# Optimization experiments

Hardware: AMD Instinct MI355X
Metric: run time of the kernel (lower is better)

Reference implementation:

```python
import jax, jax.numpy as jnp
import numpy as np

B, S, H, R, K, L = 8, 2048, 512, 7, 10, 4
OFFSETS = np.array([-3, -2, -1, 1, 2, 3], dtype=np.int32)
BN_EPS = 1e-5


def setup_inputs() -> dict:
    key = jax.random.key(0)
    ks = jax.random.split(key, 12)
    u = lambda k, shape, s: jax.random.uniform(k, shape, minval=-s, maxval=s, dtype=jnp.float32)
    s3, sh, shr = 1.0 / np.sqrt(3.0), 1.0 / np.sqrt(H), 1.0 / np.sqrt(R * H)
    return {
        "n_coords": jax.random.normal(ks[0], (B, S, 3), jnp.float32),
        "ca_coords": jax.random.normal(ks[1], (B, S, 3), jnp.float32),
        "c_coords": jax.random.normal(ks[2], (B, S, 3), jnp.float32),
        "Wp": u(ks[3], (H, 3), s3),
        "bp": u(ks[4], (H,), s3),
        "Wlin": u(ks[5], (L, H, R * H), shr),
        "blin": u(ks[6], (L, H), shr),
        "Wself": u(ks[7], (L, H, H), sh),
        "bself": u(ks[8], (L, H), sh),
        "bn_gamma": jnp.ones((L, H), jnp.float32),
        "bn_beta": jnp.zeros((L, H), jnp.float32),
        "bn_mean": jax.random.normal(ks[9], (L, H), jnp.float32) * 0.1,
        "bn_var": jax.random.uniform(ks[10], (L, H), minval=0.5, maxval=1.5, dtype=jnp.float32),
    }


def _edges(pos):
    """Edge list per graph: sequential offsets -3..3 -> relations 0..5, KNN(k=10) -> relation 6."""
    i = jnp.arange(S)
    off = jnp.asarray(OFFSETS)
    dst_seq = i[:, None] + off[None, :]                            # [S,6]
    valid = (dst_seq >= 0) & (dst_seq < S)
    src_seq = jnp.broadcast_to(i[:, None], (S, 6))
    rel_seq = jnp.broadcast_to(jnp.arange(6, dtype=jnp.int32)[None, :], (S, 6))
    dst_seq = jnp.clip(dst_seq, 0, S - 1)
    # squared distances give the same topk-smallest ordering as torch.norm
    d2 = jnp.sum((pos[:, None, :] - pos[None, :, :]) ** 2, axis=-1)  # [S,S]
    _, knn = jax.lax.top_k(-d2, K + 1)                             # k+1 smallest, self first
    dst_knn = knn[:, 1:]                                           # drop self
    src_knn = jnp.broadcast_to(i[:, None], (S, K))
    rel_knn = jnp.full((S, K), 6, dtype=jnp.int32)
    src = jnp.concatenate([src_seq.reshape(-1), src_knn.reshape(-1)])
    dst = jnp.concatenate([dst_seq.reshape(-1), dst_knn.reshape(-1)])
    rel = jnp.concatenate([rel_seq.reshape(-1), rel_knn.reshape(-1)])
    w = jnp.concatenate([valid.reshape(-1).astype(pos.dtype),
                         jnp.ones((S * K,), pos.dtype)])
    return src, dst, rel, w


def _gearnet(ca_coords, Wp, bp, Wlin, blin, Wself, bself, bn_gamma, bn_beta, bn_mean, bn_var):
    def per_graph(pos):
        src, dst, rel, w = _edges(pos)
        seg = dst * R + rel                                        # node_out*num_relation + relation
        h = pos @ Wp.T + bp                                        # coord_projection: Linear(3, H)
        for l in range(L):
            msg = h[src] * w[:, None]                              # [E,H] gather + edge weight
            upd = jax.ops.segment_sum(msg, seg, num_segments=S * R)  # scatter-add per (node, relation)
            upd = upd.reshape(S, R * H)
            out = upd @ Wlin[l].T + blin[l] + h @ Wself[l].T + bself[l]
            out = (out - bn_mean[l]) * jax.lax.rsqrt(bn_var[l] + BN_EPS) * bn_gamma[l] + bn_beta[l]
            h = jax.nn.relu(out) + h                               # relu then short_cut residual
        return h
    return jax.vmap(per_graph)(ca_coords)                          # [B,S,H]


def reference(n_coords, ca_coords, c_coords, Wp, bp, Wlin, blin, Wself, bself,
              bn_gamma, bn_beta, bn_mean, bn_var):
    # n_coords / c_coords are accepted but unused, exactly as in the original forward.
    return _gearnet(ca_coords, Wp, bp, Wlin, blin, Wself, bself,
                    bn_gamma, bn_beta, bn_mean, bn_var)
```

## Files before the change

### kernel.cpp

```cpp
#include <hip/hip_runtime.h>
#include <stdint.h>

#define B_ 8
#define S_ 2048
#define H_ 512
#define R_ 7
#define K_ 10
#define L_ 4
#define KT_ 4096
#define RH_ 3584

typedef __attribute__((ext_vector_type(8))) short bf16x8;
typedef __attribute__((ext_vector_type(4))) float f32x4;
typedef __attribute__((ext_vector_type(4))) unsigned short u16x4;
typedef unsigned long long u64;

__device__ __forceinline__ unsigned short f2bf(float f){
  unsigned int u = __float_as_uint(f);
  u = (u + 0x7fffu + ((u >> 16) & 1u)) >> 16;
  return (unsigned short)u;
}

__device__ __forceinline__ float bf2f(unsigned short s){
  return __uint_as_float(((unsigned int)s) << 16);
}

__device__ __forceinline__ f32x4 bf4load(const unsigned short* p){
  u16x4 v = *(const u16x4*)p;
  f32x4 o;
#pragma unroll
  for (int e = 0; e < 4; e++) o[e] = bf2f(v[e]);
  return o;
}

__device__ __forceinline__ void gload16(const void* g, void* lds){
  __builtin_amdgcn_global_load_lds(
      (const __attribute__((address_space(1))) unsigned int*)g,
      (__attribute__((address_space(3))) unsigned int*)lds, 16, 0, 0);
}

__global__ __launch_bounds__(256) void knn_kernel(const float* __restrict__ pos,
                                                  int* __restrict__ knn){
  __shared__ float4 p4[S_];
  int b = blockIdx.y;
  const float* p = pos + (size_t)b * S_ * 3;
  for (int idx = threadIdx.x; idx < S_; idx += 256){
    float4 v; v.x = p[idx*3+0]; v.y = p[idx*3+1]; v.z = p[idx*3+2]; v.w = 0.f;
    p4[idx] = v;
  }
  __syncthreads();
  int w = threadIdx.x >> 6, l = threadIdx.x & 63;
  int i = blockIdx.x * 4 + w;
  float4 pi = p4[i];
  float xi = pi.x, yi = pi.y, zi = pi.z;
  u64 best[6];
#pragma unroll
  for (int q = 0; q < 6; q++) best[q] = ~0ull;
#pragma unroll 1
  for (int j = l; j < S_; j += 64){
    if (j == i) continue;
    float4 pj = p4[j];
    float dx = __fsub_rn(xi, pj.x);
    float dy = __fsub_rn(yi, pj.y);
    float dz = __fsub_rn(zi, pj.z);
    float d2 = __fadd_rn(__fadd_rn(__fmul_rn(dx,dx), __fmul_rn(dy,dy)), __fmul_rn(dz,dz));
    u64 key = ((u64)__float_as_uint(d2) << 32) | (unsigned)j;
    if (key < best[5]){
      best[5] = key;
#pragma unroll
      for (int q = 5; q > 0; --q){
        u64 a = best[q-1], c = best[q];
        u64 lo = a < c ? a : c, hi = a < c ? c : a;
        best[q-1] = lo; best[q] = hi;
      }
    }
  }
  int* out = knn + ((size_t)b * S_ + i) * K_;
#pragma unroll
  for (int t = 0; t < 10; t++){
    u64 cand = best[0];
    u64 m = cand;
#pragma unroll
    for (int o = 32; o; o >>= 1){
      u64 other = __shfl_xor(m, o);
      if (other < m) m = other;
    }
    if (cand == m){
#pragma unroll
      for (int q = 0; q < 5; q++) best[q] = best[q+1];
      best[5] = ~0ull;
    }
    if (l == 0) out[t] = (int)(unsigned)(m & 0xffffffffu);
  }
}

__global__ void count_kernel(const int* __restrict__ knn, int* __restrict__ counts){
  int idx = blockIdx.x * 256 + threadIdx.x;
  int b = idx / (S_ * K_);
  int d = knn[idx];
  atomicAdd(&counts[b * S_ + d], 1);
}

__global__ __launch_bounds__(256) void scan_kernel(const int* __restrict__ counts,
                                                   int* __restrict__ row_start,
                                                   int* __restrict__ cursor){
  __shared__ int lds[256];
  int b = blockIdx.x, t = threadIdx.x;
  int base = b * S_;
  int v[8]; int s = 0;
#pragma unroll
  for (int e = 0; e < 8; e++){ v[e] = s; s += counts[base + t*8 + e]; }
  lds[t] = s;
  __syncthreads();
  int total = s;
  for (int o = 1; o < 256; o <<= 1){
    int add = 0;
    if (t >= o) add = lds[t - o];
    __syncthreads();
    lds[t] += add;
    __syncthreads();
  }
  int ex = lds[t] - total;
  int rb = b * (S_ + 1);
#pragma unroll
  for (int e = 0; e < 8; e++){
    int val = ex + v[e];
    row_start[rb + t*8 + e] = val;
    cursor[base + t*8 + e] = val;
  }
  if (t == 255) row_start[rb + S_] = lds[255];
}

__global__ void fill_kernel(const int* __restrict__ knn, int* __restrict__ cursor,
                            int* __restrict__ col){
  int idx = blockIdx.x * 256 + threadIdx.x;
  int b = idx / (S_ * K_);
  int i = (idx / K_) % S_;
  int d = knn[idx];
  int p = atomicAdd(&cursor[b * S_ + d], 1);
  col[(size_t)b * S_ * K_ + p] = i;
}

__global__ void sort_kernel(const int* __restrict__ row_start, int* __restrict__ col){
  int idx = blockIdx.x * 256 + threadIdx.x;
  int b = idx / S_, d = idx % S_;
  int rs = row_start[b*(S_+1)+d], re = row_start[b*(S_+1)+d+1];
  int* c = col + (size_t)b * S_ * K_;
  for (int a = rs + 1; a < re; ++a){
    int vv = c[a]; int q = a - 1;
    while (q >= rs && c[q] > vv){ c[q+1] = c[q]; --q; }
    c[q+1] = vv;
  }
}

__global__ void prepw_kernel(const float* __restrict__ Wlin, const float* __restrict__ Wself,
                             unsigned short* __restrict__ Wt){
  size_t e = ((size_t)blockIdx.x * 256 + threadIdx.x) * 8;
  int k = (int)(e & 4095);
  int j = (int)((e >> 12) & 511);
  int l = (int)(e >> 21);
  const float* src = (k < RH_) ? Wlin + ((size_t)l * H_ + j) * RH_ + k
                               : Wself + ((size_t)l * H_ + j) * H_ + (k - RH_);
  union { unsigned short s[8]; uint4 u; } pk;
#pragma unroll
  for (int t = 0; t < 8; t++) pk.s[t] = f2bf(src[t]);
  *(uint4*)&Wt[e] = pk.u;
}

__global__ void prepa_kernel(const float* __restrict__ gam, const float* __restrict__ bet,
                             const float* __restrict__ mean, const float* __restrict__ var,
                             const float* __restrict__ blin, const float* __restrict__ bself,
                             float* __restrict__ scale, float* __restrict__ shift){
  int idx = blockIdx.x * 256 + threadIdx.x;
  float sc = gam[idx] * rsqrtf(var[idx] + 1e-5f);
  scale[idx] = sc;
  shift[idx] = bet[idx] + (blin[idx] + bself[idx] - mean[idx]) * sc;
}

__global__ void inith_kernel(const float* __restrict__ pos, const float* __restrict__ Wp,
                             const float* __restrict__ bp, float* __restrict__ h,
                             unsigned short* __restrict__ hb){
  int idx = blockIdx.x * 256 + threadIdx.x;
  int j = (idx & 127) * 4;
  int bs = idx >> 7;
  const float* p = pos + (size_t)bs * 3;
  float x = p[0], y = p[1], z = p[2];
  f32x4 o;
#pragma unroll
  for (int e = 0; e < 4; e++){
    const float* wr = Wp + (j + e) * 3;
    o[e] = x * wr[0] + y * wr[1] + z * wr[2] + bp[j + e];
  }
  *(f32x4*)&h[(size_t)bs * H_ + j] = o;
  unsigned int w0 = f2bf(o[0]) | ((unsigned)f2bf(o[1]) << 16);
  unsigned int w1 = f2bf(o[2]) | ((unsigned)f2bf(o[3]) << 16);
  uint2 u; u.x = w0; u.y = w1;
  *(uint2*)&hb[(size_t)bs * H_ + j] = u;
}

__global__ __launch_bounds__(256) void hknn_kernel(const unsigned short* __restrict__ hb,
                                                   const int* __restrict__ row_start,
                                                   const int* __restrict__ col,
                                                   unsigned short* __restrict__ hk){
  int w = threadIdx.x >> 6, l = threadIdx.x & 63;
  int d = blockIdx.x * 4 + w;
  int b = blockIdx.y;
  int rs = row_start[b * (S_ + 1) + d];
  int re = row_start[b * (S_ + 1) + d + 1];
  const int* cl = col + (size_t)b * S_ * K_;
  const unsigned short* base = hb + (size_t)b * S_ * H_ + l * 8;
  f32x4 aLo = {0,0,0,0}, aHi = {0,0,0,0}, bLo = {0,0,0,0}, bHi = {0,0,0,0};
  int e = rs;
  for (; e + 1 < re; e += 2){
    uint4 v0 = *(const uint4*)(base + (size_t)cl[e]     * H_);
    uint4 v1 = *(const uint4*)(base + (size_t)cl[e + 1] * H_);
    aLo[0] += __uint_as_float(v0.x << 16); aLo[1] += __uint_as_float(v0.x & 0xffff0000u);
    aLo[2] += __uint_as_float(v0.y << 16); aLo[3] += __uint_as_float(v0.y & 0xffff0000u);
    aHi[0] += __uint_as_float(v0.z << 16); aHi[1] += __uint_as_float(v0.z & 0xffff0000u);
    aHi[2] += __uint_as_float(v0.w << 16); aHi[3] += __uint_as_float(v0.w & 0xffff0000u);
    bLo[0] += __uint_as_float(v1.x << 16); bLo[1] += __uint_as_float(v1.x & 0xffff0000u);
    bLo[2] += __uint_as_float(v1.y << 16); bLo[3] += __uint_as_float(v1.y & 0xffff0000u);
    bHi[0] += __uint_as_float(v1.z << 16); bHi[1] += __uint_as_float(v1.z & 0xffff0000u);
    bHi[2] += __uint_as_float(v1.w << 16); bHi[3] += __uint_as_float(v1.w & 0xffff0000u);
  }
  if (e < re){
    uint4 v0 = *(const uint4*)(base + (size_t)cl[e] * H_);
    aLo[0] += __uint_as_float(v0.x << 16); aLo[1] += __uint_as_float(v0.x & 0xffff0000u);
    aLo[2] += __uint_as_float(v0.y << 16); aLo[3] += __uint_as_float(v0.y & 0xffff0000u);
    aHi[0] += __uint_as_float(v0.z << 16); aHi[1] += __uint_as_float(v0.z & 0xffff0000u);
    aHi[2] += __uint_as_float(v0.w << 16); aHi[3] += __uint_as_float(v0.w & 0xffff0000u);
  }
  aLo += bLo; aHi += bHi;
  uint4 o;
  o.x = f2bf(aLo[0]) | ((unsigned)f2bf(aLo[1]) << 16);
  o.y = f2bf(aLo[2]) | ((unsigned)f2bf(aLo[3]) << 16);
  o.z = f2bf(aHi[0]) | ((unsigned)f2bf(aHi[1]) << 16);
  o.w = f2bf(aHi[2]) | ((unsigned)f2bf(aHi[3]) << 16);
  *(uint4*)(hk + ((size_t)b * S_ + d) * H_ + l * 8) = o;
}

__global__ __launch_bounds__(512) void gemmf_kernel(
    const unsigned short* __restrict__ hbin,
    const unsigned short* __restrict__ hkn,
    const unsigned short* __restrict__ Wt,
    float* __restrict__ h,
    unsigned short* __restrict__ hbout,
    const float* __restrict__ scale,
    const float* __restrict__ shift,
    const unsigned short* __restrict__ zbuf){
  __shared__ unsigned short As[3][128 * 64];
  __shared__ unsigned short Bs[3][256 * 64];
  int tid = threadIdx.x;
  int wg = blockIdx.x;
  int swz = (wg & 7) * 32 + (wg >> 3);
  int my = swz >> 1;
  int nx = swz & 1;
  int l = tid & 63, wid = tid >> 6;
  int wm = wid >> 2, wn = wid & 3;
  f32x4 acc[4][4] = {};

  int arow = tid >> 3;
  int lA8 = ((tid & 7) ^ (arow & 7)) << 3;
  int gr0 = my * 128 + arow, gr1 = gr0 + 64;
  const unsigned short* Bp0 = Wt + (size_t)(nx * 256 +   0 + arow) * KT_ + lA8;
  const unsigned short* Bp1 = Wt + (size_t)(nx * 256 +  64 + arow) * KT_ + lA8;
  const unsigned short* Bp2 = Wt + (size_t)(nx * 256 + 128 + arow) * KT_ + lA8;
  const unsigned short* Bp3 = Wt + (size_t)(nx * 256 + 192 + arow) * KT_ + lA8;
  const unsigned short *sa0, *sa1;

#define SETSLC(rr) do {                                                       \
    int _r = (rr);                                                            \
    const unsigned short *_b0, *_b1;                                          \
    if (_r < 6){                                                              \
      int _sh = (_r < 3) ? (3 - _r) : (2 - _r);          \
      int _s0 = gr0 + _sh, _s1 = gr1 + _sh;                                   \
      _b0 = (((unsigned)_s0 >> 11) == ((unsigned)gr0 >> 11)) ? hbin + (size_t)_s0 * H_ : zbuf; \
      _b1 = (((unsigned)_s1 >> 11) == ((unsigned)gr1 >> 11)) ? hbin + (size_t)_s1 * H_ : zbuf; \
    } else {                                                                  \
      const unsigned short* _bb = (_r == 6) ? hkn : hbin;                     \
      _b0 = _bb + (size_t)gr0 * H_; _b1 = _bb + (size_t)gr1 * H_;             \
    }                                                                         \
    sa0 = _b0 + lA8; sa1 = _b1 + lA8;                                         \
  } while (0)

  int dA0 = tid * 8, dA1 = (512 + tid) * 8;
  int dB0 = tid * 8, dB1 = (512 + tid) * 8, dB2 = (1024 + tid) * 8, dB3 = (1536 + tid) * 8;

#define STAGE(sl, ko, kb) do {                             \
    gload16(sa0 + (ko), &As[sl][dA0]);                     \
    gload16(sa1 + (ko), &As[sl][dA1]);                     \
    gload16(Bp0 + (kb), &Bs[sl][dB0]);                     \
    gload16(Bp1 + (kb), &Bs[sl][dB1]);                     \
    gload16(Bp2 + (kb), &Bs[sl][dB2]);                     \
    gload16(Bp3 + (kb), &Bs[sl][dB3]);                     \
  } while (0)

  SETSLC(0);
  STAGE(0, 0, 0);
  STAGE(1, 64, 64);
  asm volatile("s_waitcnt vmcnt(6)" ::: "memory");
  __builtin_amdgcn_s_barrier();
  asm volatile("" ::: "memory");

  int kcr = l >> 4, lr = l & 15, lr7 = l & 7;
  int rA0 = wm * 64 + lr, rB0 = wn * 64 + lr;
  int pc0 = (kcr ^ lr7) * 8;
  int pc1 = ((4 + kcr) ^ lr7) * 8;
  int s = 0;
#pragma unroll 1
  for (int t = 0; t < 64; ++t){
    int s2 = s + 2; if (s2 >= 3) s2 -= 3;
    int tt = t + 2;
    bool st = (t < 62);
    if (st) SETSLC(tt >> 3);

    bf16x8 af0[4], af1[4], bf0[4], bf1[4];
#pragma unroll
    for (int mi = 0; mi < 4; mi++)
      af0[mi] = *(const bf16x8*)&As[s][(rA0 + mi * 16) * 64 + pc0];
#pragma unroll
    for (int ni = 0; ni < 4; ni++)
      bf0[ni] = *(const bf16x8*)&Bs[s][(rB0 + ni * 16) * 64 + pc0];
    __builtin_amdgcn_sched_barrier(0);
#pragma unroll
    for (int mi = 0; mi < 4; mi++)
      af1[mi] = *(const bf16x8*)&As[s][(rA0 + mi * 16) * 64 + pc1];
#pragma unroll
    for (int ni = 0; ni < 4; ni++)
      bf1[ni] = *(const bf16x8*)&Bs[s][(rB0 + ni * 16) * 64 + pc1];
    __builtin_amdgcn_sched_barrier(0);

    asm volatile("s_waitcnt lgkmcnt(8)" ::: "memory");
    __builtin_amdgcn_sched_barrier(0);
    __builtin_amdgcn_s_setprio(1);
#pragma unroll
    for (int mi = 0; mi < 4; mi++)
#pragma unroll
      for (int ni = 0; ni < 4; ni++)
        acc[mi][ni] = __builtin_amdgcn_mfma_f32_16x16x32_bf16(af0[mi], bf0[ni], acc[mi][ni], 0, 0, 0);
    __builtin_amdgcn_s_setprio(0);
    __builtin_amdgcn_sched_barrier(0);

    if (st) STAGE(s2, (tt & 7) * 64, tt * 64);

    asm volatile("s_waitcnt lgkmcnt(0)" ::: "memory");
    __builtin_amdgcn_sched_barrier(0);
    __builtin_amdgcn_s_setprio(1);
#pragma unroll
    for (int mi = 0; mi < 4; mi++)
#pragma unroll
      for (int ni = 0; ni < 4; ni++)
        acc[mi][ni] = __builtin_amdgcn_mfma_f32_16x16x32_bf16(af1[mi], bf1[ni], acc[mi][ni], 0, 0, 0);
    __builtin_amdgcn_s_setprio(0);
    asm volatile("" ::: "memory");

    if (t < 62)       asm volatile("s_waitcnt vmcnt(6)" ::: "memory");
    else if (t == 62) asm volatile("s_waitcnt vmcnt(0)" ::: "memory");
    if (t < 63){
      __builtin_amdgcn_s_barrier();
      asm volatile("" ::: "memory");
    }
    ++s; if (s == 3) s = 0;
  }
#undef STAGE
#undef SETSLC

  int r0 = (l >> 4) * 4, c0 = l & 15;
#pragma unroll
  for (int ni = 0; ni < 4; ni++){
    int gcol = nx * 256 + wn * 64 + ni * 16 + c0;
    float sc = scale[gcol], sf = shift[gcol];
#pragma unroll
    for (int mi = 0; mi < 4; mi++){
#pragma unroll
      for (int reg = 0; reg < 4; reg++){
        int grow = my * 128 + wm * 64 + mi * 16 + r0 + reg;
        size_t o = (size_t)grow * H_ + gcol;
        float val = fmaxf(acc[mi][ni][reg] * sc + sf, 0.f);
        float hv = h[o] + val;
        h[o] = hv;
        hbout[o] = f2bf(hv);
      }
    }
  }
}

extern "C" void kernel_launch(void* const* d_in, const int* in_sizes, int n_in,
                              void* d_out, int out_size, void* d_ws, size_t ws_size,
                              hipStream_t stream){
  const float* ca    = (const float*)d_in[1];
  const float* Wp    = (const float*)d_in[3];
  const float* bp    = (const float*)d_in[4];
  const float* Wlin  = (const float*)d_in[5];
  const float* blin  = (const float*)d_in[6];
  const float* Wself = (const float*)d_in[7];
  const float* bself = (const float*)d_in[8];
  const float* gam   = (const float*)d_in[9];
  const float* bet   = (const float*)d_in[10];
  const float* mean  = (const float*)d_in[11];
  const float* var   = (const float*)d_in[12];
  float* h = (float*)d_out;

  char* ws = (char*)d_ws;
  size_t off = 0;
  auto alloc = [&](size_t bytes) -> char* {
    char* p = ws + off;
    off = (off + bytes + 255) & ~(size_t)255;
    return p;
  };
  int* knn       = (int*)alloc((size_t)B_ * S_ * K_ * 4);
  int* counts    = (int*)alloc((size_t)B_ * S_ * 4);
  int* row_start = (int*)alloc((size_t)B_ * (S_ + 1) * 4);
  int* cursor    = (int*)alloc((size_t)B_ * S_ * 4);
  int* col       = (int*)alloc((size_t)B_ * S_ * K_ * 4);
  unsigned short* Wt  = (unsigned short*)alloc((size_t)L_ * H_ * KT_ * 2);
  float* scale   = (float*)alloc((size_t)L_ * H_ * 4);
  float* shift   = (float*)alloc((size_t)L_ * H_ * 4);
  unsigned short* hbA = (unsigned short*)alloc((size_t)B_ * S_ * H_ * 2);
  unsigned short* hbB = (unsigned short*)alloc((size_t)B_ * S_ * H_ * 2);
  unsigned short* hkn = (unsigned short*)alloc((size_t)B_ * S_ * H_ * 2);
  unsigned short* zbuf = (unsigned short*)alloc(4096 * 2);

  hipMemsetAsync(counts, 0, (size_t)B_ * S_ * 4, stream);
  hipMemsetAsync(zbuf, 0, 4096 * 2, stream);
  knn_kernel<<<dim3(S_ / 4, B_), 256, 0, stream>>>(ca, knn);
  count_kernel<<<dim3(B_ * S_ * K_ / 256), 256, 0, stream>>>(knn, counts);
  scan_kernel<<<dim3(B_), 256, 0, stream>>>(counts, row_start, cursor);
  fill_kernel<<<dim3(B_ * S_ * K_ / 256), 256, 0, stream>>>(knn, cursor, col);
  sort_kernel<<<dim3(B_ * S_ / 256), 256, 0, stream>>>(row_start, col);
  prepw_kernel<<<dim3((int)((size_t)L_ * H_ * KT_ / 8 / 256)), 256, 0, stream>>>(Wlin, Wself, Wt);
  prepa_kernel<<<dim3(L_ * H_ / 256), 256, 0, stream>>>(gam, bet, mean, var, blin, bself, scale, shift);
  inith_kernel<<<dim3(B_ * S_ * (H_ / 4) / 256), 256, 0, stream>>>(ca, Wp, bp, h, hbA);

  for (int l = 0; l < L_; l++){
    unsigned short* in  = (l & 1) ? hbB : hbA;
    unsigned short* out = (l & 1) ? hbA : hbB;
    hknn_kernel<<<dim3(S_ / 4, B_), 256, 0, stream>>>(in, row_start, col, hkn);
    gemmf_kernel<<<dim3(256), 512, 0, stream>>>(
        in, hkn, Wt + (size_t)l * H_ * KT_, h, out,
        scale + l * H_, shift + l * H_, zbuf);
  }
}
```

Baseline: 527.3 us.

## Load A operand directly from global into registers, bypassing LDS

The fused GEMM now fetches the A (activation) tile straight from global memory into MFMA fragment registers with inline global_load_dwordx4, double-buffered across tiles, and keeps only the weight tile in shared memory. This drops A writes to and reads from LDS and frees LDS capacity. In exchange, A rows are read redundantly by the four wn waves through cache, register pressure rises, and the load pattern is less coalesced. The zero buffer is enlarged to cover the wider per-lane offsets.

Result: slower. 789.7 us (+49.8%).

```diff
diff --git a/kernel.cpp b/kernel.cpp
--- a/kernel.cpp
+++ b/kernel.cpp
@@ -248,7 +248,6 @@
     const float* __restrict__ scale,
     const float* __restrict__ shift,
     const unsigned short* __restrict__ zbuf){
-  __shared__ unsigned short As[3][128 * 64];
   __shared__ unsigned short Bs[3][256 * 64];
   int tid = threadIdx.x;
   int wg = blockIdx.x;
@@ -261,109 +260,120 @@
 
   int arow = tid >> 3;
   int lA8 = ((tid & 7) ^ (arow & 7)) << 3;
-  int gr0 = my * 128 + arow, gr1 = gr0 + 64;
   const unsigned short* Bp0 = Wt + (size_t)(nx * 256 +   0 + arow) * KT_ + lA8;
   const unsigned short* Bp1 = Wt + (size_t)(nx * 256 +  64 + arow) * KT_ + lA8;
   const unsigned short* Bp2 = Wt + (size_t)(nx * 256 + 128 + arow) * KT_ + lA8;
   const unsigned short* Bp3 = Wt + (size_t)(nx * 256 + 192 + arow) * KT_ + lA8;
-  const unsigned short *sa0, *sa1;
-
-#define SETSLC(rr) do {                                                       \
-    int _r = (rr);                                                            \
-    const unsigned short *_b0, *_b1;                                          \
-    if (_r < 6){                                                              \
-      int _sh = (_r < 3) ? (3 - _r) : (2 - _r);          \
-      int _s0 = gr0 + _sh, _s1 = gr1 + _sh;                                   \
-      _b0 = (((unsigned)_s0 >> 11) == ((unsigned)gr0 >> 11)) ? hbin + (size_t)_s0 * H_ : zbuf; \
-      _b1 = (((unsigned)_s1 >> 11) == ((unsigned)gr1 >> 11)) ? hbin + (size_t)_s1 * H_ : zbuf; \
-    } else {                                                                  \
-      const unsigned short* _bb = (_r == 6) ? hkn : hbin;                     \
-      _b0 = _bb + (size_t)gr0 * H_; _b1 = _bb + (size_t)gr1 * H_;             \
-    }                                                                         \
-    sa0 = _b0 + lA8; sa1 = _b1 + lA8;                                         \
-  } while (0)
-
-  int dA0 = tid * 8, dA1 = (512 + tid) * 8;
   int dB0 = tid * 8, dB1 = (512 + tid) * 8, dB2 = (1024 + tid) * 8, dB3 = (1536 + tid) * 8;
 
-#define STAGE(sl, ko, kb) do {                             \
-    gload16(sa0 + (ko), &As[sl][dA0]);                     \
-    gload16(sa1 + (ko), &As[sl][dA1]);                     \
+#define STAGEB(sl, kb) do {                                \
     gload16(Bp0 + (kb), &Bs[sl][dB0]);                     \
     gload16(Bp1 + (kb), &Bs[sl][dB1]);                     \
     gload16(Bp2 + (kb), &Bs[sl][dB2]);                     \
     gload16(Bp3 + (kb), &Bs[sl][dB3]);                     \
   } while (0)
 
+  int lr = l & 15, kcr = l >> 4, lr7 = l & 7;
+  int graphid = (my * 128) >> 11;
+  const unsigned short* pA[4];
+
+#define SETSLC(rr) do {                                                       \
+    int _r = (rr);                                                            \
+    int _sh = (_r < 6) ? ((_r < 3) ? (3 - _r) : (2 - _r)) : 0;                \
+    const unsigned short* _bb = (_r == 6) ? hkn : hbin;                       \
+    _Pragma("unroll")                                                         \
+    for (int _mi = 0; _mi < 4; _mi++){                                        \
+      int _src = my * 128 + wm * 64 + _mi * 16 + lr + _sh;                    \
+      bool _ok = (_r >= 6) || ((_src >> 11) == graphid);                      \
+      pA[_mi] = (_ok ? _bb + (size_t)_src * H_ : zbuf) + kcr * 8;             \
+    }                                                                         \
+  } while (0)
+
+#define LOADA(A, T) do {                                                      \
+    int _ko = ((T) & 7) * 64;                                                 \
+    _Pragma("unroll")                                                         \
+    for (int _mi = 0; _mi < 4; _mi++){                                        \
+      asm volatile("global_load_dwordx4 %0, %1, off"                          \
+        : "=v"(A[_mi][0]) : "v"(pA[_mi] + _ko) : "memory");                   \
+      asm volatile("global_load_dwordx4 %0, %1, off"                          \
+        : "=v"(A[_mi][1]) : "v"(pA[_mi] + _ko + 32) : "memory");              \
+    }                                                                         \
+  } while (0)
+
+  bf16x8 Ae[4][2], Ao[4][2];
+
   SETSLC(0);
-  STAGE(0, 0, 0);
-  STAGE(1, 64, 64);
-  asm volatile("s_waitcnt vmcnt(6)" ::: "memory");
+  STAGEB(0, 0);
+  STAGEB(1, 64);
+  LOADA(Ae, 0);
+  asm volatile("s_waitcnt vmcnt(12)" ::: "memory");
   __builtin_amdgcn_s_barrier();
   asm volatile("" ::: "memory");
 
-  int kcr = l >> 4, lr = l & 15, lr7 = l & 7;
-  int rA0 = wm * 64 + lr, rB0 = wn * 64 + lr;
+  int rB0 = wn * 64 + lr;
   int pc0 = (kcr ^ lr7) * 8;
   int pc1 = ((4 + kcr) ^ lr7) * 8;
   int s = 0;
+
+#define TILE(T, ACUR, ANXT) do {                                              \
+    int _t = (T);                                                             \
+    int _s2 = s + 2; if (_s2 >= 3) _s2 -= 3;                                  \
+    if (_t < 62) STAGEB(_s2, (_t + 2) * 64);                                  \
+    if (_t < 63){                                                             \
+      if (((_t + 1) & 7) == 0) SETSLC((_t + 1) >> 3);                         \
+      LOADA(ANXT, _t + 1);                                                    \
+    }                                                                         \
+    if (_t < 62)       asm volatile("s_waitcnt vmcnt(12)" ::: "memory");      \
+    else if (_t == 62) asm volatile("s_waitcnt vmcnt(8)" ::: "memory");       \
+    else               asm volatile("s_waitcnt vmcnt(0)" ::: "memory");       \
+    __builtin_amdgcn_sched_barrier(0);                                        \
+    bf16x8 _bf0[4], _bf1[4];                                                  \
+    _Pragma("unroll")                                                         \
+    for (int _ni = 0; _ni < 4; _ni++)                                         \
+      _bf0[_ni] = *(const bf16x8*)&Bs[s][(rB0 + _ni * 16) * 64 + pc0];        \
+    __builtin_amdgcn_sched_barrier(0);                                        \
+    _Pragma("unroll")                                                         \
+    for (int _ni = 0; _ni < 4; _ni++)                                         \
+      _bf1[_ni] = *(const bf16x8*)&Bs[s][(rB0 + _ni * 16) * 64 + pc1];        \
+    __builtin_amdgcn_sched_barrier(0);                                        \
+    asm volatile("s_waitcnt lgkmcnt(4)" ::: "memory");                        \
+    __builtin_amdgcn_sched_barrier(0);                                        \
+    __builtin_amdgcn_s_setprio(1);                                            \
+    _Pragma("unroll")                                                         \
+    for (int _mi = 0; _mi < 4; _mi++)                                         \
+      _Pragma("unroll")                                                       \
+      for (int _ni = 0; _ni < 4; _ni++)                                       \
+        acc[_mi][_ni] = __builtin_amdgcn_mfma_f32_16x16x32_bf16(              \
+            ACUR[_mi][0], _bf0[_ni], acc[_mi][_ni], 0, 0, 0);                 \
+    __builtin_amdgcn_s_setprio(0);                                            \
+    __builtin_amdgcn_sched_barrier(0);                                        \
+    asm volatile("s_waitcnt lgkmcnt(0)" ::: "memory");                        \
+    __builtin_amdgcn_sched_barrier(0);                                        \
+    __builtin_amdgcn_s_setprio(1);                                            \
+    _Pragma("unroll")                                                         \
+    for (int _mi = 0; _mi < 4; _mi++)                                         \
+      _Pragma("unroll")                                                       \
+      for (int _ni = 0; _ni < 4; _ni++)                                       \
+        acc[_mi][_ni] = __builtin_amdgcn_mfma_f32_16x16x32_bf16(              \
+            ACUR[_mi][1], _bf1[_ni], acc[_mi][_ni], 0, 0, 0);                 \
+    __builtin_amdgcn_s_setprio(0);                                            \
+    asm volatile("" ::: "memory");                                            \
+    if (_t < 63){                                                             \
+      __builtin_amdgcn_s_barrier();                                           \
+      asm volatile("" ::: "memory");                                          \
+    }                                                                         \
+    ++s; if (s == 3) s = 0;                                                   \
+  } while (0)
+
 #pragma unroll 1
-  for (int t = 0; t < 64; ++t){
-    int s2 = s + 2; if (s2 >= 3) s2 -= 3;
-    int tt = t + 2;
-    bool st = (t < 62);
-    if (st) SETSLC(tt >> 3);
-
-    bf16x8 af0[4], af1[4], bf0[4], bf1[4];
-#pragma unroll
-    for (int mi = 0; mi < 4; mi++)
-      af0[mi] = *(const bf16x8*)&As[s][(rA0 + mi * 16) * 64 + pc0];
-#pragma unroll
-    for (int ni = 0; ni < 4; ni++)
-      bf0[ni] = *(const bf16x8*)&Bs[s][(rB0 + ni * 16) * 64 + pc0];
-    __builtin_amdgcn_sched_barrier(0);
-#pragma unroll
-    for (int mi = 0; mi < 4; mi++)
-      af1[mi] = *(const bf16x8*)&As[s][(rA0 + mi * 16) * 64 + pc1];
-#pragma unroll
-    for (int ni = 0; ni < 4; ni++)
-      bf1[ni] = *(const bf16x8*)&Bs[s][(rB0 + ni * 16) * 64 + pc1];
-    __builtin_amdgcn_sched_barrier(0);
-
-    asm volatile("s_waitcnt lgkmcnt(8)" ::: "memory");
-    __builtin_amdgcn_sched_barrier(0);
-    __builtin_amdgcn_s_setprio(1);
-#pragma unroll
-    for (int mi = 0; mi < 4; mi++)
-#pragma unroll
-      for (int ni = 0; ni < 4; ni++)
-        acc[mi][ni] = __builtin_amdgcn_mfma_f32_16x16x32_bf16(af0[mi], bf0[ni], acc[mi][ni], 0, 0, 0);
-    __builtin_amdgcn_s_setprio(0);
-    __builtin_amdgcn_sched_barrier(0);
-
-    if (st) STAGE(s2, (tt & 7) * 64, tt * 64);
-
-    asm volatile("s_waitcnt lgkmcnt(0)" ::: "memory");
-    __builtin_amdgcn_sched_barrier(0);
-    __builtin_amdgcn_s_setprio(1);
-#pragma unroll
-    for (int mi = 0; mi < 4; mi++)
-#pragma unroll
-      for (int ni = 0; ni < 4; ni++)
-        acc[mi][ni] = __builtin_amdgcn_mfma_f32_16x16x32_bf16(af1[mi], bf1[ni], acc[mi][ni], 0, 0, 0);
-    __builtin_amdgcn_s_setprio(0);
-    asm volatile("" ::: "memory");
-
-    if (t < 62)       asm volatile("s_waitcnt vmcnt(6)" ::: "memory");
-    else if (t == 62) asm volatile("s_waitcnt vmcnt(0)" ::: "memory");
-    if (t < 63){
-      __builtin_amdgcn_s_barrier();
-      asm volatile("" ::: "memory");
-    }
-    ++s; if (s == 3) s = 0;
-  }
-#undef STAGE
+  for (int tp = 0; tp < 32; ++tp){
+    TILE(2 * tp,     Ae, Ao);
+    TILE(2 * tp + 1, Ao, Ae);
+  }
+#undef TILE
+#undef LOADA
 #undef SETSLC
+#undef STAGEB
 
   int r0 = (l >> 4) * 4, c0 = l & 15;
 #pragma unroll
@@ -419,10 +429,10 @@
   unsigned short* hbA = (unsigned short*)alloc((size_t)B_ * S_ * H_ * 2);
   unsigned short* hbB = (unsigned short*)alloc((size_t)B_ * S_ * H_ * 2);
   unsigned short* hkn = (unsigned short*)alloc((size_t)B_ * S_ * H_ * 2);
-  unsigned short* zbuf = (unsigned short*)alloc(4096 * 2);
+  unsigned short* zbuf = (unsigned short*)alloc(8192 * 2);
 
   hipMemsetAsync(counts, 0, (size_t)B_ * S_ * 4, stream);
-  hipMemsetAsync(zbuf, 0, 4096 * 2, stream);
+  hipMemsetAsync(zbuf, 0, 8192 * 2, stream);
   knn_kernel<<<dim3(S_ / 4, B_), 256, 0, stream>>>(ca, knn);
   count_kernel<<<dim3(B_ * S_ * K_ / 256), 256, 0, stream>>>(knn, counts);
   scan_kernel<<<dim3(B_), 256, 0, stream>>>(counts, row_start, cursor);
```

## Retile fused GEMM to 128x128 blocks with K=32 steps and 4-stage pipeline

Applied to the files above, without the earlier changes.

The fused relation GEMM moves from 128x256 tiles with 512 threads and a 3-stage, 64-wide K pipeline to 128x128 tiles with 256 threads, 32-wide K steps and a 4-stage LDS ring. The grid doubles to 512 workgroups and the LDS swizzle is redone for the narrower rows. The aim is better occupancy and CU coverage on a 256-CU part, plus a deeper prefetch. In exchange, A-tile reuse drops so the activation operand is loaded twice as often, and there are twice as many barriers per K.

Measured after the change: 568.8 us. 7.9% more time.

```diff
diff --git a/kernel.cpp b/kernel.cpp
--- a/kernel.cpp
+++ b/kernel.cpp
@@ -239,7 +239,7 @@
   *(uint4*)(hk + ((size_t)b * S_ + d) * H_ + l * 8) = o;
 }
 
-__global__ __launch_bounds__(512) void gemmf_kernel(
+__global__ __launch_bounds__(256) void gemmf_kernel(
     const unsigned short* __restrict__ hbin,
     const unsigned short* __restrict__ hkn,
     const unsigned short* __restrict__ Wt,
@@ -248,24 +248,23 @@
     const float* __restrict__ scale,
     const float* __restrict__ shift,
     const unsigned short* __restrict__ zbuf){
-  __shared__ unsigned short As[3][128 * 64];
-  __shared__ unsigned short Bs[3][256 * 64];
+  __shared__ unsigned short As[4][128 * 32];
+  __shared__ unsigned short Bs[4][128 * 32];
   int tid = threadIdx.x;
   int wg = blockIdx.x;
-  int swz = (wg & 7) * 32 + (wg >> 3);
-  int my = swz >> 1;
-  int nx = swz & 1;
+  int swz = (wg & 7) * 64 + (wg >> 3);
+  int my = swz >> 2;
+  int nx = swz & 3;
   int l = tid & 63, wid = tid >> 6;
-  int wm = wid >> 2, wn = wid & 3;
+  int wm = wid >> 1, wn = wid & 1;
   f32x4 acc[4][4] = {};
 
-  int arow = tid >> 3;
-  int lA8 = ((tid & 7) ^ (arow & 7)) << 3;
+  int arow = tid >> 2;
+  int kc = (tid & 3) ^ ((arow >> 1) & 3);
+  int lA8 = kc << 3;
   int gr0 = my * 128 + arow, gr1 = gr0 + 64;
-  const unsigned short* Bp0 = Wt + (size_t)(nx * 256 +   0 + arow) * KT_ + lA8;
-  const unsigned short* Bp1 = Wt + (size_t)(nx * 256 +  64 + arow) * KT_ + lA8;
-  const unsigned short* Bp2 = Wt + (size_t)(nx * 256 + 128 + arow) * KT_ + lA8;
-  const unsigned short* Bp3 = Wt + (size_t)(nx * 256 + 192 + arow) * KT_ + lA8;
+  const unsigned short* Bp0 = Wt + (size_t)(nx * 128 + arow) * KT_ + lA8;
+  const unsigned short* Bp1 = Wt + (size_t)(nx * 128 + arow + 64) * KT_ + lA8;
   const unsigned short *sa0, *sa1;
 
 #define SETSLC(rr) do {                                                       \
@@ -283,65 +282,49 @@
     sa0 = _b0 + lA8; sa1 = _b1 + lA8;                                         \
   } while (0)
 
-  int dA0 = tid * 8, dA1 = (512 + tid) * 8;
-  int dB0 = tid * 8, dB1 = (512 + tid) * 8, dB2 = (1024 + tid) * 8, dB3 = (1536 + tid) * 8;
+  int dA0 = tid * 8, dA1 = (256 + tid) * 8;
 
 #define STAGE(sl, ko, kb) do {                             \
     gload16(sa0 + (ko), &As[sl][dA0]);                     \
     gload16(sa1 + (ko), &As[sl][dA1]);                     \
-    gload16(Bp0 + (kb), &Bs[sl][dB0]);                     \
-    gload16(Bp1 + (kb), &Bs[sl][dB1]);                     \
-    gload16(Bp2 + (kb), &Bs[sl][dB2]);                     \
-    gload16(Bp3 + (kb), &Bs[sl][dB3]);                     \
+    gload16(Bp0 + (kb), &Bs[sl][dA0]);                     \
+    gload16(Bp1 + (kb), &Bs[sl][dA1]);                     \
   } while (0)
 
   SETSLC(0);
   STAGE(0, 0, 0);
-  STAGE(1, 64, 64);
-  asm volatile("s_waitcnt vmcnt(6)" ::: "memory");
+  STAGE(1, 32, 32);
+  STAGE(2, 64, 64);
+  asm volatile("s_waitcnt vmcnt(8)" ::: "memory");
   __builtin_amdgcn_s_barrier();
   asm volatile("" ::: "memory");
 
-  int kcr = l >> 4, lr = l & 15, lr7 = l & 7;
+  int kcr = l >> 4, lr = l & 15;
   int rA0 = wm * 64 + lr, rB0 = wn * 64 + lr;
-  int pc0 = (kcr ^ lr7) * 8;
-  int pc1 = ((4 + kcr) ^ lr7) * 8;
   int s = 0;
 #pragma unroll 1
-  for (int t = 0; t < 64; ++t){
-    int s2 = s + 2; if (s2 >= 3) s2 -= 3;
-    int tt = t + 2;
-    bool st = (t < 62);
-    if (st) SETSLC(tt >> 3);
-
-    bf16x8 af0[4], af1[4], bf0[4], bf1[4];
-#pragma unroll
-    for (int mi = 0; mi < 4; mi++)
-      af0[mi] = *(const bf16x8*)&As[s][(rA0 + mi * 16) * 64 + pc0];
-#pragma unroll
-    for (int ni = 0; ni < 4; ni++)
-      bf0[ni] = *(const bf16x8*)&Bs[s][(rB0 + ni * 16) * 64 + pc0];
+  for (int t = 0; t < 128; ++t){
+    int s3 = (s + 3) & 3;
+    int tt = t + 3;
+    bool st = (t < 125);
+    if (st && (tt & 15) == 0) SETSLC(tt >> 4);
+
+    bf16x8 af[4], bf[4];
+#pragma unroll
+    for (int mi = 0; mi < 4; mi++){
+      int row = rA0 + mi * 16;
+      int slot = kcr ^ ((row >> 1) & 3);
+      af[mi] = *(const bf16x8*)&As[s][row * 32 + slot * 8];
+    }
+#pragma unroll
+    for (int ni = 0; ni < 4; ni++){
+      int row = rB0 + ni * 16;
+      int slot = kcr ^ ((row >> 1) & 3);
+      bf[ni] = *(const bf16x8*)&Bs[s][row * 32 + slot * 8];
+    }
     __builtin_amdgcn_sched_barrier(0);
-#pragma unroll
-    for (int mi = 0; mi < 4; mi++)
-      af1[mi] = *(const bf16x8*)&As[s][(rA0 + mi * 16) * 64 + pc1];
-#pragma unroll
-    for (int ni = 0; ni < 4; ni++)
-      bf1[ni] = *(const bf16x8*)&Bs[s][(rB0 + ni * 16) * 64 + pc1];
-    __builtin_amdgcn_sched_barrier(0);
-
-    asm volatile("s_waitcnt lgkmcnt(8)" ::: "memory");
-    __builtin_amdgcn_sched_barrier(0);
-    __builtin_amdgcn_s_setprio(1);
-#pragma unroll
-    for (int mi = 0; mi < 4; mi++)
-#pragma unroll
-      for (int ni = 0; ni < 4; ni++)
-        acc[mi][ni] = __builtin_amdgcn_mfma_f32_16x16x32_bf16(af0[mi], bf0[ni], acc[mi][ni], 0, 0, 0);
-    __builtin_amdgcn_s_setprio(0);
-    __builtin_amdgcn_sched_barrier(0);
-
-    if (st) STAGE(s2, (tt & 7) * 64, tt * 64);
+
+    if (st) STAGE(s3, (tt & 15) * 32, tt * 32);
 
     asm volatile("s_waitcnt lgkmcnt(0)" ::: "memory");
     __builtin_amdgcn_sched_barrier(0);
@@ -350,17 +333,18 @@
     for (int mi = 0; mi < 4; mi++)
 #pragma unroll
       for (int ni = 0; ni < 4; ni++)
-        acc[mi][ni] = __builtin_amdgcn_mfma_f32_16x16x32_bf16(af1[mi], bf1[ni], acc[mi][ni], 0, 0, 0);
+        acc[mi][ni] = __builtin_amdgcn_mfma_f32_16x16x32_bf16(af[mi], bf[ni], acc[mi][ni], 0, 0, 0);
     __builtin_amdgcn_s_setprio(0);
     asm volatile("" ::: "memory");
 
-    if (t < 62)       asm volatile("s_waitcnt vmcnt(6)" ::: "memory");
-    else if (t == 62) asm volatile("s_waitcnt vmcnt(0)" ::: "memory");
-    if (t < 63){
+    if (st)            asm volatile("s_waitcnt vmcnt(8)" ::: "memory");
+    else if (t == 125) asm volatile("s_waitcnt vmcnt(4)" ::: "memory");
+    else if (t == 126) asm volatile("s_waitcnt vmcnt(0)" ::: "memory");
+    if (t < 127){
       __builtin_amdgcn_s_barrier();
       asm volatile("" ::: "memory");
     }
-    ++s; if (s == 3) s = 0;
+    s = (s + 1) & 3;
   }
 #undef STAGE
 #undef SETSLC
@@ -368,7 +352,7 @@
   int r0 = (l >> 4) * 4, c0 = l & 15;
 #pragma unroll
   for (int ni = 0; ni < 4; ni++){
-    int gcol = nx * 256 + wn * 64 + ni * 16 + c0;
+    int gcol = nx * 128 + wn * 64 + ni * 16 + c0;
     float sc = scale[gcol], sf = shift[gcol];
 #pragma unroll
     for (int mi = 0; mi < 4; mi++){
@@ -436,7 +420,7 @@
     unsigned short* in  = (l & 1) ? hbB : hbA;
     unsigned short* out = (l & 1) ? hbA : hbB;
     hknn_kernel<<<dim3(S_ / 4, B_), 256, 0, stream>>>(in, row_start, col, hkn);
-    gemmf_kernel<<<dim3(256), 512, 0, stream>>>(
+    gemmf_kernel<<<dim3(512), 256, 0, stream>>>(
         in, hkn, Wt + (size_t)l * H_ * KT_, h, out,
         scale + l * H_, shift + l * H_, zbuf);
   }
```
